# Optimization experiments

Hardware: AMD Instinct MI355X
Metric: run time of the kernel (lower is better)

Reference implementation:

```python
import jax, jax.numpy as jnp
import numpy as np


def setup_inputs() -> dict:
    key = jax.random.key(0)
    k1, k2, k3, k4, k5 = jax.random.split(key, 5)
    B, N, M, D = 4096, 2048, 2048, 9
    return {
        "x": jax.random.normal(k1, (B, N), dtype=jnp.float32),
        "eternal_weights": jax.random.normal(k2, (D, N, M), dtype=jnp.float32),
        "eternal_biases": jax.random.normal(k3, (M,), dtype=jnp.float32),
        "classical_weights": jax.random.normal(k4, (N, M), dtype=jnp.float32),
        "classical_biases": jax.random.normal(k5, (M,), dtype=jnp.float32),
    }


def _eternal_probs(eternal_weights, n, m):
    # The gate matrix is cos*I - sin*P + sin*P^T with P the circular shift,
    # so (gate @ s)[i] = cos*s[i] - sin*s[(i+1)%n] + sin*s[(i-1)%n].
    # Vectorize over all m output units at once: state is [m, n].
    state0 = jnp.full((m, n), 1.0 / np.sqrt(n), dtype=eternal_weights.dtype)
    angles = eternal_weights[:, :m, :3]  # [D, m, 3] -- weights[depth, j, 0/1/2]

    def gate(state, angle):  # angle: [m]
        c = jnp.cos(angle)[:, None]
        s = jnp.sin(angle)[:, None]
        return c * state - s * jnp.roll(state, -1, axis=1) + s * jnp.roll(state, 1, axis=1)

    def step(state, ang):  # ang: [m, 3] -- consciousness, intelligence, wisdom
        state = gate(state, ang[:, 0])
        state = gate(state, ang[:, 1])
        state = gate(state, ang[:, 2])
        return state, None

    state, _ = jax.lax.scan(step, state0, angles)
    return jnp.abs(state[:, 0]) ** 2  # [m]


def reference(x, eternal_weights, eternal_biases, classical_weights, classical_biases):
    # eternal_biases exists as a parameter in the original module but is unused in forward.
    n = x.shape[1]
    m = classical_weights.shape[1]
    classical = x @ classical_weights + classical_biases  # [B, m]
    probs = _eternal_probs(eternal_weights, n, m)  # [m], identical for every batch row
    return jnp.tanh(classical + probs[None, :])
```

## Files before the change

kernel.cpp:

```cpp
#include <hip/hip_runtime.h>
#include <hip/hip_fp8.h>
#include <stdint.h>

static constexpr int MM = 4096;
static constexpr int KK = 2048;
static constexpr int NN = 2048;

typedef float floatx16 __attribute__((ext_vector_type(16)));
typedef __bf16 bf16x8 __attribute__((ext_vector_type(8)));
typedef unsigned short u16x8 __attribute__((ext_vector_type(8)));
typedef int intx4 __attribute__((ext_vector_type(4)));
typedef int intx8 __attribute__((ext_vector_type(8)));
typedef unsigned char u8x16 __attribute__((ext_vector_type(16)));

__device__ __forceinline__ unsigned short bf16_rne(float x) {
  union { float f; uint32_t u; } c; c.f = x;
  uint32_t u = c.u;
  u += 0x7fffu + ((u >> 16) & 1u);
  return (unsigned short)(u >> 16);
}
__device__ __forceinline__ float bf16_as_f32(unsigned short h) {
  union { float f; uint32_t u; } c; c.u = ((uint32_t)h) << 16;
  return c.f;
}
__device__ __forceinline__ unsigned char f32_to_e4m3(float x) {
  __hip_fp8_e4m3 q(x);
  return (unsigned char)q.__x;
}
__device__ __forceinline__ float fast_tanh(float x) {
  float e = __expf(2.0f * x);
  return 1.0f - 2.0f / (e + 1.0f);
}
__device__ __forceinline__ float bflo(unsigned int w) {
  union { float f; unsigned u; } c; c.u = w << 16; return c.f;
}
__device__ __forceinline__ float bfhi(unsigned int w) {
  union { float f; unsigned u; } c; c.u = w & 0xffff0000u; return c.f;
}


__global__ __launch_bounds__(256) void prepass_kernel(
    const float* __restrict__ x, const float* __restrict__ E,
    const float* __restrict__ W, const float* __restrict__ cb,
    unsigned short* __restrict__ ahi, unsigned char* __restrict__ al8,
    unsigned short* __restrict__ bhi, unsigned char* __restrict__ bl8,
    float* __restrict__ bias2) {
  __shared__ float tile[64][65];
  const int blk = blockIdx.x;
  const int tid = threadIdx.x;

  if (blk < 2048) {
    int idx = blk * 256 + tid;
    int row = idx >> 7;
    int u = idx & 127;
    int g = u >> 2;
    int q = u & 3;
    const float4* s = (const float4*)(x + (size_t)row * KK + u * 16);
    float v[16];
#pragma unroll
    for (int p = 0; p < 4; p++) {
      float4 t = s[p];
      v[p * 4 + 0] = t.x; v[p * 4 + 1] = t.y; v[p * 4 + 2] = t.z; v[p * 4 + 3] = t.w;
    }
    unsigned short h[16];
    union { unsigned char b[16]; unsigned long long d[2]; } loq;
#pragma unroll
    for (int e = 0; e < 16; e++) {
      h[e] = bf16_rne(v[e]);
      float lo = v[e] - bf16_as_f32(h[e]);
      loq.b[e] = f32_to_e4m3(lo * 512.0f);
    }
    size_t rb = (size_t)row * KK;
#pragma unroll
    for (int cc = 0; cc < 2; cc++) {
      int c8 = q * 2 + cc;
      int phys8 = (c8 + row + (row >> 3)) & 7;
      u16x8 o;
#pragma unroll
      for (int e = 0; e < 8; e++) o[e] = h[cc * 8 + e];
      *(u16x8*)(ahi + rb + g * 64 + phys8 * 8) = o;
    }
    {
      int sw = (row & 3) + ((row >> 2) & 3);
      int cA = (q >> 1) * 2;
      char* lb = (char*)al8 + rb + g * 64;
      *(unsigned long long*)(lb + (((cA + 0) + sw) & 3) * 16 + (q & 1) * 8) = loq.d[0];
      *(unsigned long long*)(lb + (((cA + 1) + sw) & 3) * 16 + (q & 1) * 8) = loq.d[1];
    }
  } else if (blk < 3072) {
    const int wb = blk - 2048;
    const int n0 = (wb & 31) * 64;
    const int k0 = (wb >> 5) * 64;
#pragma unroll
    for (int i = 0; i < 4; i++) {
      int t = tid + i * 256;
      int kr = t >> 4;
      int nc = (t & 15) * 4;
      const float4 vv = *(const float4*)(W + (size_t)(k0 + kr) * NN + n0 + nc);
      tile[nc + 0][kr] = vv.x;
      tile[nc + 1][kr] = vv.y;
      tile[nc + 2][kr] = vv.z;
      tile[nc + 3][kr] = vv.w;
    }
    __syncthreads();
    const int nl = tid >> 2;
    const int q = tid & 3;
    const int n = n0 + nl;
    float v[16];
    unsigned short h[16];
    union { unsigned char b[16]; unsigned long long d[2]; } loq;
#pragma unroll
    for (int e = 0; e < 16; e++) {
      v[e] = tile[nl][q * 16 + e];
      h[e] = bf16_rne(v[e]);
      float lo = v[e] - bf16_as_f32(h[e]);
      loq.b[e] = f32_to_e4m3(lo * 512.0f);
    }
    size_t rb = (size_t)n * KK + k0;
#pragma unroll
    for (int cc = 0; cc < 2; cc++) {
      int c8 = q * 2 + cc;
      int phys8 = (c8 + n + (n >> 3)) & 7;
      u16x8 o;
#pragma unroll
      for (int e = 0; e < 8; e++) o[e] = h[cc * 8 + e];
      *(u16x8*)(bhi + rb + phys8 * 8) = o;
    }
    {
      int sw = (n & 3) + ((n >> 2) & 3);
      int cA = (q >> 1) * 2;
      char* lb = (char*)bl8 + rb;
      *(unsigned long long*)(lb + (((cA + 0) + sw) & 3) * 16 + (q & 1) * 8) = loq.d[0];
      *(unsigned long long*)(lb + (((cA + 1) + sw) & 3) * 16 + (q & 1) * 8) = loq.d[1];
    }
  } else {
    int i = (blk - 3072) * 256 + tid;
    if (i < NN) {
      float p = 1.0f / 2048.0f;
#pragma unroll
      for (int d = 0; d < 9; d++) {
        const float4 a = *(const float4*)(E + (size_t)d * (2048 * 2048) + (size_t)i * 2048);
        float c0 = cosf(a.x), c1 = cosf(a.y), c2 = cosf(a.z);
        p *= (c0 * c0) * (c1 * c1) * (c2 * c2);
      }
      bias2[i] = cb[i] + p;
    }
  }
}

#define GLL(dst, src)                                                        \
  __builtin_amdgcn_global_load_lds(                                          \
      (const __attribute__((address_space(1))) void*)(src),                  \
      (__attribute__((address_space(3))) void*)(dst), 16, 0, 0)

__global__ __launch_bounds__(256, 2) void gemm_tanh_kernel(
    const unsigned short* __restrict__ Ahi, const unsigned char* __restrict__ Al8,
    const unsigned short* __restrict__ Bhi, const unsigned char* __restrict__ Bl8,
    const float* __restrict__ bias2, float* __restrict__ out) {
  __shared__ __align__(16) unsigned short sAh[2][128 * 64];
  __shared__ __align__(16) unsigned short sBh[2][128 * 64];
  __shared__ __align__(16) unsigned char sAl[128 * 64];
  __shared__ __align__(16) unsigned char sBl[128 * 64];

  const int tid = threadIdx.x;
  const int lane = tid & 63;
  const int wave = tid >> 6;
  const int wm = (wave >> 1) * 64;
  const int wn = (wave & 1) * 64;

  const int id = blockIdx.x;
  const int cid = id >> 4, lid = id & 15;
  const int bm = ((cid >> 2) * 4 + (lid >> 2)) * 128;
  const int bn = ((cid & 3) * 4 + (lid & 3)) * 128;

  const size_t a16 = (size_t)(bm + (tid >> 3)) * KK + (tid & 7) * 8;
  const size_t b16 = (size_t)(bn + (tid >> 3)) * KK + (tid & 7) * 8;
  const size_t a8b = (size_t)(bm + (tid >> 2)) * KK + (tid & 3) * 16;
  const size_t b8b = (size_t)(bn + (tid >> 2)) * KK + (tid & 3) * 16;
  const int lds16 = tid * 8;
  const int lds8 = tid * 16;

  const int r31 = lane & 31;
  const int half = lane >> 5;

  floatx16 acc[2][2];
#pragma unroll
  for (int i = 0; i < 2; i++)
#pragma unroll
    for (int j = 0; j < 2; j++)
#pragma unroll
      for (int r = 0; r < 16; r++) acc[i][j][r] = 0.f;

#pragma unroll
  for (int p = 0; p < 4; p++) {
    GLL(&sAh[0][p * 2048 + lds16], Ahi + a16 + (size_t)(32 * p) * KK);
    GLL(&sBh[0][p * 2048 + lds16], Bhi + b16 + (size_t)(32 * p) * KK);
  }

  for (int kt = 0; kt < 32; ++kt) {
    const int k0 = kt * 64;
    const int cur = kt & 1;
    const int nxt = cur ^ 1;

    __builtin_amdgcn_s_barrier();
    __builtin_amdgcn_sched_barrier(0);
#pragma unroll
    for (int p = 0; p < 2; p++) {
      GLL(&sAl[p * 4096 + lds8], Al8 + a8b + (size_t)k0 + (size_t)(64 * p) * KK);
      GLL(&sBl[p * 4096 + lds8], Bl8 + b8b + (size_t)k0 + (size_t)(64 * p) * KK);
    }
    const size_t kn = (kt < 31) ? (size_t)(k0 + 64) : 0;
#pragma unroll
    for (int p = 0; p < 4; p++) {
      GLL(&sAh[nxt][p * 2048 + lds16], Ahi + a16 + kn + (size_t)(32 * p) * KK);
      GLL(&sBh[nxt][p * 2048 + lds16], Bhi + b16 + kn + (size_t)(32 * p) * KK);
    }
    asm volatile("s_waitcnt vmcnt(12)" ::: "memory");
    __builtin_amdgcn_sched_barrier(0);
    __builtin_amdgcn_s_barrier();
    __builtin_amdgcn_sched_barrier(0);

    intx8 fa8[2], fb8[2];
#pragma unroll
    for (int s = 0; s < 4; s++) {
      const int c8 = s * 2 + half;
      bf16x8 fa[2], fb[2];
#pragma unroll
      for (int t = 0; t < 2; t++) {
        int rowA = wm + t * 32 + r31;
        int ao = rowA * 64 + ((c8 + rowA + (rowA >> 3)) & 7) * 8;
        fa[t] = *(const bf16x8*)(&sAh[cur][ao]);
        int rowB = wn + t * 32 + r31;
        int bo = rowB * 64 + ((c8 + rowB + (rowB >> 3)) & 7) * 8;
        fb[t] = *(const bf16x8*)(&sBh[cur][bo]);
      }
#pragma unroll
      for (int i = 0; i < 2; i++)
#pragma unroll
        for (int j = 0; j < 2; j++)
          acc[i][j] = __builtin_amdgcn_mfma_f32_32x32x16_bf16(fa[i], fb[j], acc[i][j], 0, 0, 0);
#pragma unroll
      for (int t = 0; t < 2; t++) {
        uint4 ua = *(const uint4*)&fa[t];
        int d0 = __builtin_amdgcn_cvt_pk_fp8_f32(bflo(ua.x), bfhi(ua.x), 0, false);
        d0 = __builtin_amdgcn_cvt_pk_fp8_f32(bflo(ua.y), bfhi(ua.y), d0, true);
        int d1 = __builtin_amdgcn_cvt_pk_fp8_f32(bflo(ua.z), bfhi(ua.z), 0, false);
        d1 = __builtin_amdgcn_cvt_pk_fp8_f32(bflo(ua.w), bfhi(ua.w), d1, true);
        fa8[t][2 * s] = d0; fa8[t][2 * s + 1] = d1;
        uint4 ub = *(const uint4*)&fb[t];
        int e0 = __builtin_amdgcn_cvt_pk_fp8_f32(bflo(ub.x), bfhi(ub.x), 0, false);
        e0 = __builtin_amdgcn_cvt_pk_fp8_f32(bflo(ub.y), bfhi(ub.y), e0, true);
        int e1 = __builtin_amdgcn_cvt_pk_fp8_f32(bflo(ub.z), bfhi(ub.z), 0, false);
        e1 = __builtin_amdgcn_cvt_pk_fp8_f32(bflo(ub.w), bfhi(ub.w), e1, true);
        fb8[t][2 * s] = e0; fb8[t][2 * s + 1] = e1;
      }
    }

    asm volatile("s_waitcnt vmcnt(8)" ::: "memory");
    __builtin_amdgcn_sched_barrier(0);
    __builtin_amdgcn_s_barrier();
    __builtin_amdgcn_sched_barrier(0);

    intx8 fal[2], fbl[2];
#pragma unroll
    for (int t = 0; t < 2; t++) {
      int rowA = wm + t * 32 + r31;
      int swA = (rowA & 3) + ((rowA >> 2) & 3);
      ((intx4*)&fal[t])[0] = *(const intx4*)(&sAl[rowA * 64 + ((half + swA) & 3) * 16]);
      ((intx4*)&fal[t])[1] = *(const intx4*)(&sAl[rowA * 64 + ((2 + half + swA) & 3) * 16]);
      int rowB = wn + t * 32 + r31;
      int swB = (rowB & 3) + ((rowB >> 2) & 3);
      ((intx4*)&fbl[t])[0] = *(const intx4*)(&sBl[rowB * 64 + ((half + swB) & 3) * 16]);
      ((intx4*)&fbl[t])[1] = *(const intx4*)(&sBl[rowB * 64 + ((2 + half + swB) & 3) * 16]);
    }
#pragma unroll
    for (int i = 0; i < 2; i++)
#pragma unroll
      for (int j = 0; j < 2; j++)
        acc[i][j] = __builtin_amdgcn_mfma_scale_f32_32x32x64_f8f6f4(
            fal[i], fb8[j], acc[i][j], 0, 0, 0, 0x76767676, 0, 0x7f7f7f7f);
#pragma unroll
    for (int i = 0; i < 2; i++)
#pragma unroll
      for (int j = 0; j < 2; j++)
        acc[i][j] = __builtin_amdgcn_mfma_scale_f32_32x32x64_f8f6f4(
            fa8[i], fbl[j], acc[i][j], 0, 0, 0, 0x7f7f7f7f, 0, 0x76767676);
  }

#pragma unroll
  for (int j = 0; j < 2; j++) {
    int col = bn + wn + j * 32 + r31;
    float b2 = bias2[col];
#pragma unroll
    for (int i = 0; i < 2; i++) {
      int row0 = bm + wm + i * 32 + 4 * half;
#pragma unroll
      for (int r = 0; r < 16; r++) {
        int row = row0 + (r & 3) + 8 * (r >> 2);
        float val = acc[i][j][r] + b2;
        __builtin_nontemporal_store(fast_tanh(val), &out[(size_t)row * NN + col]);
      }
    }
  }
}

__global__ __launch_bounds__(256) void fallback_gemm(
    const float* __restrict__ x, const float* __restrict__ E,
    const float* __restrict__ W, const float* __restrict__ cb,
    float* __restrict__ out) {
  __shared__ float sA[16][16];
  __shared__ float sB[16][17];
  __shared__ float sbias[16];
  const int tx = threadIdx.x, ty = threadIdx.y;
  const int row = blockIdx.y * 16 + ty;
  const int col = blockIdx.x * 16 + tx;
  if (ty == 0) {
    float p = 1.0f / 2048.0f;
    for (int d = 0; d < 9; d++) {
      const float* a = E + (size_t)d * (2048 * 2048) + (size_t)col * 2048;
      for (int t = 0; t < 3; t++) { float c = cosf(a[t]); p *= c * c; }
    }
    sbias[tx] = p + cb[col];
  }
  float acc = 0.f;
  for (int k0 = 0; k0 < KK; k0 += 16) {
    __syncthreads();
    sA[ty][tx] = x[(size_t)row * KK + k0 + tx];
    sB[ty][tx] = W[(size_t)(k0 + ty) * NN + col];
    __syncthreads();
#pragma unroll
    for (int kk = 0; kk < 16; kk++) acc += sA[ty][kk] * sB[kk][tx];
  }
  out[(size_t)row * NN + col] = tanhf(acc + sbias[tx]);
}

extern "C" void kernel_launch(void* const* d_in, const int* in_sizes, int n_in,
                              void* d_out, int out_size, void* d_ws, size_t ws_size,
                              hipStream_t stream) {
  const float* x  = (const float*)d_in[0];
  const float* E  = (const float*)d_in[1];
  const float* W  = (const float*)d_in[3];
  const float* cb = (const float*)d_in[4];
  float* out = (float*)d_out;

  const size_t MB = 1024 * 1024;
  const size_t need = 36 * MB + NN * sizeof(float);
  if (ws_size < need) {
    fallback_gemm<<<dim3(NN / 16, MM / 16), dim3(16, 16), 0, stream>>>(x, E, W, cb, out);
    return;
  }

  char* ws = (char*)d_ws;
  unsigned short* Ahi = (unsigned short*)(ws);
  unsigned short* Bhi = (unsigned short*)(ws + 16 * MB);
  unsigned char* Al8  = (unsigned char*)(ws + 24 * MB);
  unsigned char* Bl8  = (unsigned char*)(ws + 32 * MB);
  float* bias2 = (float*)(ws + 36 * MB);

  prepass_kernel<<<dim3(3080), dim3(256), 0, stream>>>(
      x, E, W, cb, Ahi, Al8, Bhi, Bl8, bias2);
  gemm_tanh_kernel<<<dim3(512), dim3(256), 0, stream>>>(
      Ahi, Al8, Bhi, Bl8, bias2, out);
}
```

Measured before the change: 308.3 us.

## Switch split-precision GEMM from bf16 to fp16 hi part with perm-based fp8 cross terms

Replaces the bf16 high part with fp16 and rescales the fp8 residual (x2048, scale exponent adjusted). The cross-term operands are now taken as the high byte of each fp16 via byte permutes, read as the bf8 format, instead of eight cvt_pk_fp8 conversions per fragment. The change also unrolls the k-loop by two with static buffer indices, precomputes LDS offsets, and raises wave priority around the MFMA sections. This aims to cut VALU conversion and address work in the inner loop, at the risk of fp16 range and accuracy limits.

```diff
diff --git a/kernel.cpp b/kernel.cpp
--- a/kernel.cpp
+++ b/kernel.cpp
@@ -7,22 +7,11 @@
 static constexpr int NN = 2048;
 
 typedef float floatx16 __attribute__((ext_vector_type(16)));
-typedef __bf16 bf16x8 __attribute__((ext_vector_type(8)));
+typedef _Float16 f16x8 __attribute__((ext_vector_type(8)));
 typedef unsigned short u16x8 __attribute__((ext_vector_type(8)));
 typedef int intx4 __attribute__((ext_vector_type(4)));
 typedef int intx8 __attribute__((ext_vector_type(8)));
-typedef unsigned char u8x16 __attribute__((ext_vector_type(16)));
-
-__device__ __forceinline__ unsigned short bf16_rne(float x) {
-  union { float f; uint32_t u; } c; c.f = x;
-  uint32_t u = c.u;
-  u += 0x7fffu + ((u >> 16) & 1u);
-  return (unsigned short)(u >> 16);
-}
-__device__ __forceinline__ float bf16_as_f32(unsigned short h) {
-  union { float f; uint32_t u; } c; c.u = ((uint32_t)h) << 16;
-  return c.f;
-}
+
 __device__ __forceinline__ unsigned char f32_to_e4m3(float x) {
   __hip_fp8_e4m3 q(x);
   return (unsigned char)q.__x;
@@ -31,11 +20,13 @@
   float e = __expf(2.0f * x);
   return 1.0f - 2.0f / (e + 1.0f);
 }
-__device__ __forceinline__ float bflo(unsigned int w) {
-  union { float f; unsigned u; } c; c.u = w << 16; return c.f;
-}
-__device__ __forceinline__ float bfhi(unsigned int w) {
-  union { float f; unsigned u; } c; c.u = w & 0xffff0000u; return c.f;
+__device__ __forceinline__ unsigned short f32_to_f16_bits(float x) {
+  union { _Float16 h; unsigned short u; } c; c.h = (_Float16)x;
+  return c.u;
+}
+__device__ __forceinline__ float f16_bits_to_f32(unsigned short u) {
+  union { _Float16 h; unsigned short u; } c; c.u = u;
+  return (float)c.h;
 }
 
 
@@ -66,9 +57,9 @@
     union { unsigned char b[16]; unsigned long long d[2]; } loq;
 #pragma unroll
     for (int e = 0; e < 16; e++) {
-      h[e] = bf16_rne(v[e]);
-      float lo = v[e] - bf16_as_f32(h[e]);
-      loq.b[e] = f32_to_e4m3(lo * 512.0f);
+      h[e] = f32_to_f16_bits(v[e]);
+      float lo = v[e] - f16_bits_to_f32(h[e]);
+      loq.b[e] = f32_to_e4m3(lo * 2048.0f);
     }
     size_t rb = (size_t)row * KK;
 #pragma unroll
@@ -112,9 +103,9 @@
 #pragma unroll
     for (int e = 0; e < 16; e++) {
       v[e] = tile[nl][q * 16 + e];
-      h[e] = bf16_rne(v[e]);
-      float lo = v[e] - bf16_as_f32(h[e]);
-      loq.b[e] = f32_to_e4m3(lo * 512.0f);
+      h[e] = f32_to_f16_bits(v[e]);
+      float lo = v[e] - f16_bits_to_f32(h[e]);
+      loq.b[e] = f32_to_e4m3(lo * 2048.0f);
     }
     size_t rb = (size_t)n * KK + k0;
 #pragma unroll
@@ -153,14 +144,74 @@
       (const __attribute__((address_space(1))) void*)(src),                  \
       (__attribute__((address_space(3))) void*)(dst), 16, 0, 0)
 
+#define BODY(CUR, NXT, KLO, KNX)                                               \
+  {                                                                            \
+    __builtin_amdgcn_s_barrier();                                              \
+    __builtin_amdgcn_sched_barrier(0);                                         \
+    _Pragma("unroll") for (int p = 0; p < 2; p++) {                            \
+      GLL(&sAl[p * 4096 + lds8], Al8 + a8b + (size_t)(KLO) + (size_t)(64 * p) * KK); \
+      GLL(&sBl[p * 4096 + lds8], Bl8 + b8b + (size_t)(KLO) + (size_t)(64 * p) * KK); \
+    }                                                                          \
+    _Pragma("unroll") for (int p = 0; p < 4; p++) {                            \
+      GLL(&sAh[NXT][p * 2048 + lds16], Ahi + a16 + (size_t)(KNX) + (size_t)(32 * p) * KK); \
+      GLL(&sBh[NXT][p * 2048 + lds16], Bhi + b16 + (size_t)(KNX) + (size_t)(32 * p) * KK); \
+    }                                                                          \
+    asm volatile("s_waitcnt vmcnt(12)" ::: "memory");                          \
+    __builtin_amdgcn_sched_barrier(0);                                         \
+    __builtin_amdgcn_s_barrier();                                              \
+    __builtin_amdgcn_sched_barrier(0);                                         \
+    intx8 fa8[2], fb8[2];                                                      \
+    __builtin_amdgcn_s_setprio(1);                                             \
+    _Pragma("unroll") for (int s = 0; s < 4; s++) {                            \
+      f16x8 fa[2], fb[2];                                                      \
+      _Pragma("unroll") for (int t = 0; t < 2; t++) {                          \
+        fa[t] = *(const f16x8*)(sAhB + (CUR) * 16384 + aho[s][t]);             \
+        fb[t] = *(const f16x8*)(sBhB + (CUR) * 16384 + bho[s][t]);             \
+      }                                                                        \
+      _Pragma("unroll") for (int i = 0; i < 2; i++)                            \
+        _Pragma("unroll") for (int j = 0; j < 2; j++)                          \
+          acc[i][j] = __builtin_amdgcn_mfma_f32_32x32x16_f16(fa[i], fb[j], acc[i][j], 0, 0, 0); \
+      _Pragma("unroll") for (int t = 0; t < 2; t++) {                          \
+        const uint4 ua = *(const uint4*)&fa[t];                                \
+        fa8[t][2 * s]     = (int)__builtin_amdgcn_perm(ua.y, ua.x, 0x07050301u); \
+        fa8[t][2 * s + 1] = (int)__builtin_amdgcn_perm(ua.w, ua.z, 0x07050301u); \
+        const uint4 ub = *(const uint4*)&fb[t];                                \
+        fb8[t][2 * s]     = (int)__builtin_amdgcn_perm(ub.y, ub.x, 0x07050301u); \
+        fb8[t][2 * s + 1] = (int)__builtin_amdgcn_perm(ub.w, ub.z, 0x07050301u); \
+      }                                                                        \
+    }                                                                          \
+    __builtin_amdgcn_s_setprio(0);                                             \
+    asm volatile("s_waitcnt vmcnt(8)" ::: "memory");                           \
+    __builtin_amdgcn_sched_barrier(0);                                         \
+    __builtin_amdgcn_s_barrier();                                              \
+    __builtin_amdgcn_sched_barrier(0);                                         \
+    intx8 fal[2], fbl[2];                                                      \
+    _Pragma("unroll") for (int t = 0; t < 2; t++) {                            \
+      ((intx4*)&fal[t])[0] = *(const intx4*)(sAlB + alo[t][0]);                \
+      ((intx4*)&fal[t])[1] = *(const intx4*)(sAlB + alo[t][1]);                \
+      ((intx4*)&fbl[t])[0] = *(const intx4*)(sBlB + blo[t][0]);                \
+      ((intx4*)&fbl[t])[1] = *(const intx4*)(sBlB + blo[t][1]);                \
+    }                                                                          \
+    __builtin_amdgcn_s_setprio(1);                                             \
+    _Pragma("unroll") for (int i = 0; i < 2; i++)                              \
+      _Pragma("unroll") for (int j = 0; j < 2; j++)                            \
+        acc[i][j] = __builtin_amdgcn_mfma_scale_f32_32x32x64_f8f6f4(           \
+            fal[i], fb8[j], acc[i][j], 0, 1, 0, 0x74747474, 0, 0x7f7f7f7f);    \
+    _Pragma("unroll") for (int i = 0; i < 2; i++)                              \
+      _Pragma("unroll") for (int j = 0; j < 2; j++)                            \
+        acc[i][j] = __builtin_amdgcn_mfma_scale_f32_32x32x64_f8f6f4(           \
+            fa8[i], fbl[j], acc[i][j], 1, 0, 0, 0x7f7f7f7f, 0, 0x74747474);    \
+    __builtin_amdgcn_s_setprio(0);                                             \
+  }
+
 __global__ __launch_bounds__(256, 2) void gemm_tanh_kernel(
     const unsigned short* __restrict__ Ahi, const unsigned char* __restrict__ Al8,
     const unsigned short* __restrict__ Bhi, const unsigned char* __restrict__ Bl8,
     const float* __restrict__ bias2, float* __restrict__ out) {
-  __shared__ __align__(16) unsigned short sAh[2][128 * 64];
-  __shared__ __align__(16) unsigned short sBh[2][128 * 64];
-  __shared__ __align__(16) unsigned char sAl[128 * 64];
-  __shared__ __align__(16) unsigned char sBl[128 * 64];
+  __shared__ __align__(16) unsigned short sAh[2][8192];
+  __shared__ __align__(16) unsigned short sBh[2][8192];
+  __shared__ __align__(16) unsigned char sAl[8192];
+  __shared__ __align__(16) unsigned char sBl[8192];
 
   const int tid = threadIdx.x;
   const int lane = tid & 63;
@@ -183,6 +234,33 @@
   const int r31 = lane & 31;
   const int half = lane >> 5;
 
+  const char* sAhB = (const char*)(&sAh[0][0]);
+  const char* sBhB = (const char*)(&sBh[0][0]);
+  const char* sAlB = (const char*)(&sAl[0]);
+  const char* sBlB = (const char*)(&sBl[0]);
+  int aho[4][2], bho[4][2];
+#pragma unroll
+  for (int s = 0; s < 4; s++)
+#pragma unroll
+    for (int t = 0; t < 2; t++) {
+      const int rowA = wm + t * 32 + r31;
+      aho[s][t] = rowA * 128 + ((2 * s + half + rowA + (rowA >> 3)) & 7) * 16;
+      const int rowB = wn + t * 32 + r31;
+      bho[s][t] = rowB * 128 + ((2 * s + half + rowB + (rowB >> 3)) & 7) * 16;
+    }
+  int alo[2][2], blo[2][2];
+#pragma unroll
+  for (int t = 0; t < 2; t++) {
+    const int rowA = wm + t * 32 + r31;
+    const int swA = (rowA & 3) + ((rowA >> 2) & 3);
+    alo[t][0] = rowA * 64 + ((half + swA) & 3) * 16;
+    alo[t][1] = rowA * 64 + ((2 + half + swA) & 3) * 16;
+    const int rowB = wn + t * 32 + r31;
+    const int swB = (rowB & 3) + ((rowB >> 2) & 3);
+    blo[t][0] = rowB * 64 + ((half + swB) & 3) * 16;
+    blo[t][1] = rowB * 64 + ((2 + half + swB) & 3) * 16;
+  }
+
   floatx16 acc[2][2];
 #pragma unroll
   for (int i = 0; i < 2; i++)
@@ -197,95 +275,12 @@
     GLL(&sBh[0][p * 2048 + lds16], Bhi + b16 + (size_t)(32 * p) * KK);
   }
 
-  for (int kt = 0; kt < 32; ++kt) {
+  for (int kt = 0; kt < 32; kt += 2) {
     const int k0 = kt * 64;
-    const int cur = kt & 1;
-    const int nxt = cur ^ 1;
-
-    __builtin_amdgcn_s_barrier();
-    __builtin_amdgcn_sched_barrier(0);
-#pragma unroll
-    for (int p = 0; p < 2; p++) {
-      GLL(&sAl[p * 4096 + lds8], Al8 + a8b + (size_t)k0 + (size_t)(64 * p) * KK);
-      GLL(&sBl[p * 4096 + lds8], Bl8 + b8b + (size_t)k0 + (size_t)(64 * p) * KK);
-    }
-    const size_t kn = (kt < 31) ? (size_t)(k0 + 64) : 0;
-#pragma unroll
-    for (int p = 0; p < 4; p++) {
-      GLL(&sAh[nxt][p * 2048 + lds16], Ahi + a16 + kn + (size_t)(32 * p) * KK);
-      GLL(&sBh[nxt][p * 2048 + lds16], Bhi + b16 + kn + (size_t)(32 * p) * KK);
-    }
-    asm volatile("s_waitcnt vmcnt(12)" ::: "memory");
-    __builtin_amdgcn_sched_barrier(0);
-    __builtin_amdgcn_s_barrier();
-    __builtin_amdgcn_sched_barrier(0);
-
-    intx8 fa8[2], fb8[2];
-#pragma unroll
-    for (int s = 0; s < 4; s++) {
-      const int c8 = s * 2 + half;
-      bf16x8 fa[2], fb[2];
-#pragma unroll
-      for (int t = 0; t < 2; t++) {
-        int rowA = wm + t * 32 + r31;
-        int ao = rowA * 64 + ((c8 + rowA + (rowA >> 3)) & 7) * 8;
-        fa[t] = *(const bf16x8*)(&sAh[cur][ao]);
-        int rowB = wn + t * 32 + r31;
-        int bo = rowB * 64 + ((c8 + rowB + (rowB >> 3)) & 7) * 8;
-        fb[t] = *(const bf16x8*)(&sBh[cur][bo]);
-      }
-#pragma unroll
-      for (int i = 0; i < 2; i++)
-#pragma unroll
-        for (int j = 0; j < 2; j++)
-          acc[i][j] = __builtin_amdgcn_mfma_f32_32x32x16_bf16(fa[i], fb[j], acc[i][j], 0, 0, 0);
-#pragma unroll
-      for (int t = 0; t < 2; t++) {
-        uint4 ua = *(const uint4*)&fa[t];
-        int d0 = __builtin_amdgcn_cvt_pk_fp8_f32(bflo(ua.x), bfhi(ua.x), 0, false);
-        d0 = __builtin_amdgcn_cvt_pk_fp8_f32(bflo(ua.y), bfhi(ua.y), d0, true);
-        int d1 = __builtin_amdgcn_cvt_pk_fp8_f32(bflo(ua.z), bfhi(ua.z), 0, false);
-        d1 = __builtin_amdgcn_cvt_pk_fp8_f32(bflo(ua.w), bfhi(ua.w), d1, true);
-        fa8[t][2 * s] = d0; fa8[t][2 * s + 1] = d1;
-        uint4 ub = *(const uint4*)&fb[t];
-        int e0 = __builtin_amdgcn_cvt_pk_fp8_f32(bflo(ub.x), bfhi(ub.x), 0, false);
-        e0 = __builtin_amdgcn_cvt_pk_fp8_f32(bflo(ub.y), bfhi(ub.y), e0, true);
-        int e1 = __builtin_amdgcn_cvt_pk_fp8_f32(bflo(ub.z), bfhi(ub.z), 0, false);
-        e1 = __builtin_amdgcn_cvt_pk_fp8_f32(bflo(ub.w), bfhi(ub.w), e1, true);
-        fb8[t][2 * s] = e0; fb8[t][2 * s + 1] = e1;
-      }
-    }
-
-    asm volatile("s_waitcnt vmcnt(8)" ::: "memory");
-    __builtin_amdgcn_sched_barrier(0);
-    __builtin_amdgcn_s_barrier();
-    __builtin_amdgcn_sched_barrier(0);
-
-    intx8 fal[2], fbl[2];
-#pragma unroll
-    for (int t = 0; t < 2; t++) {
-      int rowA = wm + t * 32 + r31;
-      int swA = (rowA & 3) + ((rowA >> 2) & 3);
-      ((intx4*)&fal[t])[0] = *(const intx4*)(&sAl[rowA * 64 + ((half + swA) & 3) * 16]);
-      ((intx4*)&fal[t])[1] = *(const intx4*)(&sAl[rowA * 64 + ((2 + half + swA) & 3) * 16]);
-      int rowB = wn + t * 32 + r31;
-      int swB = (rowB & 3) + ((rowB >> 2) & 3);
-      ((intx4*)&fbl[t])[0] = *(const intx4*)(&sBl[rowB * 64 + ((half + swB) & 3) * 16]);
-      ((intx4*)&fbl[t])[1] = *(const intx4*)(&sBl[rowB * 64 + ((2 + half + swB) & 3) * 16]);
-    }
-#pragma unroll
-    for (int i = 0; i < 2; i++)
-#pragma unroll
-      for (int j = 0; j < 2; j++)
-        acc[i][j] = __builtin_amdgcn_mfma_scale_f32_32x32x64_f8f6f4(
-            fal[i], fb8[j], acc[i][j], 0, 0, 0, 0x76767676, 0, 0x7f7f7f7f);
-#pragma unroll
-    for (int i = 0; i < 2; i++)
-#pragma unroll
-      for (int j = 0; j < 2; j++)
-        acc[i][j] = __builtin_amdgcn_mfma_scale_f32_32x32x64_f8f6f4(
-            fa8[i], fbl[j], acc[i][j], 0, 0, 0, 0x7f7f7f7f, 0, 0x76767676);
-  }
+    BODY(0, 1, k0, k0 + 64)
+    BODY(1, 0, k0 + 64, (kt < 30) ? (k0 + 128) : 0)
+  }
+  asm volatile("s_waitcnt vmcnt(0)" ::: "memory");
 
 #pragma unroll
   for (int j = 0; j < 2; j++) {
```

After: 295.0 us. -4.3%, faster.

## Switch to fp16 hi split with MFMA-fragment layout and direct global loads

Applied to the files above, without the earlier changes.

The prepass now splits inputs into fp16 high parts plus e4m3 residuals scaled by 2048, and writes them in a tiled layout that matches the MFMA fragment order. The GEMM kernel drops the LDS staging and barriers and loads fragments straight from global memory into registers. It also gets the fp8 copy of the high part by byte-permuting fp16 into bf8 instead of running float conversions, and raises wave priority around the MFMA blocks. The risks are the loss of prefetch double-buffering, which can expose global latency, and the narrower fp16 exponent range for the high part.

```diff
diff --git a/kernel.cpp b/kernel.cpp
--- a/kernel.cpp
+++ b/kernel.cpp
@@ -7,22 +7,11 @@
 static constexpr int NN = 2048;
 
 typedef float floatx16 __attribute__((ext_vector_type(16)));
-typedef __bf16 bf16x8 __attribute__((ext_vector_type(8)));
+typedef _Float16 f16x8 __attribute__((ext_vector_type(8)));
 typedef unsigned short u16x8 __attribute__((ext_vector_type(8)));
 typedef int intx4 __attribute__((ext_vector_type(4)));
 typedef int intx8 __attribute__((ext_vector_type(8)));
-typedef unsigned char u8x16 __attribute__((ext_vector_type(16)));
-
-__device__ __forceinline__ unsigned short bf16_rne(float x) {
-  union { float f; uint32_t u; } c; c.f = x;
-  uint32_t u = c.u;
-  u += 0x7fffu + ((u >> 16) & 1u);
-  return (unsigned short)(u >> 16);
-}
-__device__ __forceinline__ float bf16_as_f32(unsigned short h) {
-  union { float f; uint32_t u; } c; c.u = ((uint32_t)h) << 16;
-  return c.f;
-}
+
 __device__ __forceinline__ unsigned char f32_to_e4m3(float x) {
   __hip_fp8_e4m3 q(x);
   return (unsigned char)q.__x;
@@ -31,11 +20,13 @@
   float e = __expf(2.0f * x);
   return 1.0f - 2.0f / (e + 1.0f);
 }
-__device__ __forceinline__ float bflo(unsigned int w) {
-  union { float f; unsigned u; } c; c.u = w << 16; return c.f;
-}
-__device__ __forceinline__ float bfhi(unsigned int w) {
-  union { float f; unsigned u; } c; c.u = w & 0xffff0000u; return c.f;
+__device__ __forceinline__ unsigned short f32_to_f16_bits(float x) {
+  union { _Float16 h; unsigned short u; } c; c.h = (_Float16)x;
+  return c.u;
+}
+__device__ __forceinline__ float f16_bits_to_f32(unsigned short u) {
+  union { _Float16 h; unsigned short u; } c; c.u = u;
+  return (float)c.h;
 }
 
 
@@ -66,31 +57,29 @@
     union { unsigned char b[16]; unsigned long long d[2]; } loq;
 #pragma unroll
     for (int e = 0; e < 16; e++) {
-      h[e] = bf16_rne(v[e]);
-      float lo = v[e] - bf16_as_f32(h[e]);
-      loq.b[e] = f32_to_e4m3(lo * 512.0f);
-    }
-    size_t rb = (size_t)row * KK;
+      h[e] = f32_to_f16_bits(v[e]);
+      float lo = v[e] - f16_bits_to_f32(h[e]);
+      loq.b[e] = f32_to_e4m3(lo * 2048.0f);
+    }
+    char* ah = (char*)ahi + (size_t)(row >> 5) * 131072 + (size_t)g * 4096 + (row & 31) * 16;
 #pragma unroll
     for (int cc = 0; cc < 2; cc++) {
-      int c8 = q * 2 + cc;
-      int phys8 = (c8 + row + (row >> 3)) & 7;
       u16x8 o;
 #pragma unroll
       for (int e = 0; e < 8; e++) o[e] = h[cc * 8 + e];
-      *(u16x8*)(ahi + rb + g * 64 + phys8 * 8) = o;
+      *(u16x8*)(ah + (2 * q + cc) * 512) = o;
     }
     {
-      int sw = (row & 3) + ((row >> 2) & 3);
-      int cA = (q >> 1) * 2;
-      char* lb = (char*)al8 + rb + g * 64;
-      *(unsigned long long*)(lb + (((cA + 0) + sw) & 3) * 16 + (q & 1) * 8) = loq.d[0];
-      *(unsigned long long*)(lb + (((cA + 1) + sw) & 3) * 16 + (q & 1) * 8) = loq.d[1];
+      char* al = (char*)al8 + (size_t)(row >> 5) * 65536 + (size_t)g * 2048 +
+                 (row & 31) * 16 + (q & 1) * 8;
+      *(unsigned long long*)(al + (q & 2) * 512) = loq.d[0];
+      *(unsigned long long*)(al + ((q & 2) | 1) * 512) = loq.d[1];
     }
   } else if (blk < 3072) {
     const int wb = blk - 2048;
     const int n0 = (wb & 31) * 64;
     const int k0 = (wb >> 5) * 64;
+    const int g = wb >> 5;
 #pragma unroll
     for (int i = 0; i < 4; i++) {
       int t = tid + i * 256;
@@ -112,26 +101,23 @@
 #pragma unroll
     for (int e = 0; e < 16; e++) {
       v[e] = tile[nl][q * 16 + e];
-      h[e] = bf16_rne(v[e]);
-      float lo = v[e] - bf16_as_f32(h[e]);
-      loq.b[e] = f32_to_e4m3(lo * 512.0f);
-    }
-    size_t rb = (size_t)n * KK + k0;
+      h[e] = f32_to_f16_bits(v[e]);
+      float lo = v[e] - f16_bits_to_f32(h[e]);
+      loq.b[e] = f32_to_e4m3(lo * 2048.0f);
+    }
+    char* bh = (char*)bhi + (size_t)(n >> 5) * 131072 + (size_t)g * 4096 + (n & 31) * 16;
 #pragma unroll
     for (int cc = 0; cc < 2; cc++) {
-      int c8 = q * 2 + cc;
-      int phys8 = (c8 + n + (n >> 3)) & 7;
       u16x8 o;
 #pragma unroll
       for (int e = 0; e < 8; e++) o[e] = h[cc * 8 + e];
-      *(u16x8*)(bhi + rb + phys8 * 8) = o;
+      *(u16x8*)(bh + (2 * q + cc) * 512) = o;
     }
     {
-      int sw = (n & 3) + ((n >> 2) & 3);
-      int cA = (q >> 1) * 2;
-      char* lb = (char*)bl8 + rb;
-      *(unsigned long long*)(lb + (((cA + 0) + sw) & 3) * 16 + (q & 1) * 8) = loq.d[0];
-      *(unsigned long long*)(lb + (((cA + 1) + sw) & 3) * 16 + (q & 1) * 8) = loq.d[1];
+      char* bl = (char*)bl8 + (size_t)(n >> 5) * 65536 + (size_t)g * 2048 +
+                 (n & 31) * 16 + (q & 1) * 8;
+      *(unsigned long long*)(bl + (q & 2) * 512) = loq.d[0];
+      *(unsigned long long*)(bl + ((q & 2) | 1) * 512) = loq.d[1];
     }
   } else {
     int i = (blk - 3072) * 256 + tid;
@@ -148,20 +134,13 @@
   }
 }
 
-#define GLL(dst, src)                                                        \
-  __builtin_amdgcn_global_load_lds(                                          \
-      (const __attribute__((address_space(1))) void*)(src),                  \
-      (__attribute__((address_space(3))) void*)(dst), 16, 0, 0)
+#define GLDH(p) (*(const __attribute__((address_space(1))) f16x8*)(p))
+#define GLD4(p) (*(const __attribute__((address_space(1))) intx4*)(p))
 
 __global__ __launch_bounds__(256, 2) void gemm_tanh_kernel(
     const unsigned short* __restrict__ Ahi, const unsigned char* __restrict__ Al8,
     const unsigned short* __restrict__ Bhi, const unsigned char* __restrict__ Bl8,
     const float* __restrict__ bias2, float* __restrict__ out) {
-  __shared__ __align__(16) unsigned short sAh[2][128 * 64];
-  __shared__ __align__(16) unsigned short sBh[2][128 * 64];
-  __shared__ __align__(16) unsigned char sAl[128 * 64];
-  __shared__ __align__(16) unsigned char sBl[128 * 64];
-
   const int tid = threadIdx.x;
   const int lane = tid & 63;
   const int wave = tid >> 6;
@@ -173,16 +152,20 @@
   const int bm = ((cid >> 2) * 4 + (lid >> 2)) * 128;
   const int bn = ((cid & 3) * 4 + (lid & 3)) * 128;
 
-  const size_t a16 = (size_t)(bm + (tid >> 3)) * KK + (tid & 7) * 8;
-  const size_t b16 = (size_t)(bn + (tid >> 3)) * KK + (tid & 7) * 8;
-  const size_t a8b = (size_t)(bm + (tid >> 2)) * KK + (tid & 3) * 16;
-  const size_t b8b = (size_t)(bn + (tid >> 2)) * KK + (tid & 3) * 16;
-  const int lds16 = tid * 8;
-  const int lds8 = tid * 16;
-
   const int r31 = lane & 31;
   const int half = lane >> 5;
 
+  const char* aH[2]; const char* bH[2]; const char* aL[2]; const char* bL[2];
+#pragma unroll
+  for (int t = 0; t < 2; t++) {
+    const size_t Ta = (size_t)((bm + wm + 32 * t) >> 5);
+    aH[t] = (const char*)Ahi + Ta * 131072 + half * 512 + r31 * 16;
+    aL[t] = (const char*)Al8 + Ta * 65536 + half * 512 + r31 * 16;
+    const size_t Tb = (size_t)((bn + wn + 32 * t) >> 5);
+    bH[t] = (const char*)Bhi + Tb * 131072 + half * 512 + r31 * 16;
+    bL[t] = (const char*)Bl8 + Tb * 65536 + half * 512 + r31 * 16;
+  }
+
   floatx16 acc[2][2];
 #pragma unroll
   for (int i = 0; i < 2; i++)
@@ -191,100 +174,75 @@
 #pragma unroll
       for (int r = 0; r < 16; r++) acc[i][j][r] = 0.f;
 
-#pragma unroll
-  for (int p = 0; p < 4; p++) {
-    GLL(&sAh[0][p * 2048 + lds16], Ahi + a16 + (size_t)(32 * p) * KK);
-    GLL(&sBh[0][p * 2048 + lds16], Bhi + b16 + (size_t)(32 * p) * KK);
-  }
-
-  for (int kt = 0; kt < 32; ++kt) {
-    const int k0 = kt * 64;
-    const int cur = kt & 1;
-    const int nxt = cur ^ 1;
-
-    __builtin_amdgcn_s_barrier();
-    __builtin_amdgcn_sched_barrier(0);
-#pragma unroll
-    for (int p = 0; p < 2; p++) {
-      GLL(&sAl[p * 4096 + lds8], Al8 + a8b + (size_t)k0 + (size_t)(64 * p) * KK);
-      GLL(&sBl[p * 4096 + lds8], Bl8 + b8b + (size_t)k0 + (size_t)(64 * p) * KK);
-    }
-    const size_t kn = (kt < 31) ? (size_t)(k0 + 64) : 0;
-#pragma unroll
-    for (int p = 0; p < 4; p++) {
-      GLL(&sAh[nxt][p * 2048 + lds16], Ahi + a16 + kn + (size_t)(32 * p) * KK);
-      GLL(&sBh[nxt][p * 2048 + lds16], Bhi + b16 + kn + (size_t)(32 * p) * KK);
-    }
-    asm volatile("s_waitcnt vmcnt(12)" ::: "memory");
-    __builtin_amdgcn_sched_barrier(0);
-    __builtin_amdgcn_s_barrier();
-    __builtin_amdgcn_sched_barrier(0);
+  for (int g = 0; g < 32; ++g) {
+    f16x8 fa[4][2], fb[4][2];
+#pragma unroll
+    for (int s = 0; s < 4; s++)
+#pragma unroll
+      for (int t = 0; t < 2; t++) {
+        fa[s][t] = GLDH(aH[t] + s * 1024);
+        fb[s][t] = GLDH(bH[t] + s * 1024);
+      }
+    intx4 la[2][2], lb[2][2];
+#pragma unroll
+    for (int t = 0; t < 2; t++)
+#pragma unroll
+      for (int c = 0; c < 2; c++) {
+        la[t][c] = GLD4(aL[t] + c * 1024);
+        lb[t][c] = GLD4(bL[t] + c * 1024);
+      }
+
+    __builtin_amdgcn_s_setprio(1);
+#pragma unroll
+    for (int s = 0; s < 4; s++)
+#pragma unroll
+      for (int i = 0; i < 2; i++)
+#pragma unroll
+        for (int j = 0; j < 2; j++)
+          acc[i][j] = __builtin_amdgcn_mfma_f32_32x32x16_f16(fa[s][i], fb[s][j], acc[i][j], 0, 0, 0);
+    __builtin_amdgcn_s_setprio(0);
 
     intx8 fa8[2], fb8[2];
 #pragma unroll
-    for (int s = 0; s < 4; s++) {
-      const int c8 = s * 2 + half;
-      bf16x8 fa[2], fb[2];
+    for (int s = 0; s < 4; s++)
 #pragma unroll
       for (int t = 0; t < 2; t++) {
-        int rowA = wm + t * 32 + r31;
-        int ao = rowA * 64 + ((c8 + rowA + (rowA >> 3)) & 7) * 8;
-        fa[t] = *(const bf16x8*)(&sAh[cur][ao]);
-        int rowB = wn + t * 32 + r31;
-        int bo = rowB * 64 + ((c8 + rowB + (rowB >> 3)) & 7) * 8;
-        fb[t] = *(const bf16x8*)(&sBh[cur][bo]);
-      }
-#pragma unroll
-      for (int i = 0; i < 2; i++)
-#pragma unroll
-        for (int j = 0; j < 2; j++)
-          acc[i][j] = __builtin_amdgcn_mfma_f32_32x32x16_bf16(fa[i], fb[j], acc[i][j], 0, 0, 0);
-#pragma unroll
-      for (int t = 0; t < 2; t++) {
-        uint4 ua = *(const uint4*)&fa[t];
-        int d0 = __builtin_amdgcn_cvt_pk_fp8_f32(bflo(ua.x), bfhi(ua.x), 0, false);
-        d0 = __builtin_amdgcn_cvt_pk_fp8_f32(bflo(ua.y), bfhi(ua.y), d0, true);
-        int d1 = __builtin_amdgcn_cvt_pk_fp8_f32(bflo(ua.z), bfhi(ua.z), 0, false);
-        d1 = __builtin_amdgcn_cvt_pk_fp8_f32(bflo(ua.w), bfhi(ua.w), d1, true);
-        fa8[t][2 * s] = d0; fa8[t][2 * s + 1] = d1;
-        uint4 ub = *(const uint4*)&fb[t];
-        int e0 = __builtin_amdgcn_cvt_pk_fp8_f32(bflo(ub.x), bfhi(ub.x), 0, false);
-        e0 = __builtin_amdgcn_cvt_pk_fp8_f32(bflo(ub.y), bfhi(ub.y), e0, true);
-        int e1 = __builtin_amdgcn_cvt_pk_fp8_f32(bflo(ub.z), bfhi(ub.z), 0, false);
-        e1 = __builtin_amdgcn_cvt_pk_fp8_f32(bflo(ub.w), bfhi(ub.w), e1, true);
-        fb8[t][2 * s] = e0; fb8[t][2 * s + 1] = e1;
-      }
-    }
-
-    asm volatile("s_waitcnt vmcnt(8)" ::: "memory");
-    __builtin_amdgcn_sched_barrier(0);
-    __builtin_amdgcn_s_barrier();
-    __builtin_amdgcn_sched_barrier(0);
-
+        const uint4 ua = *(const uint4*)&fa[s][t];
+        fa8[t][2 * s]     = (int)__builtin_amdgcn_perm(ua.y, ua.x, 0x07050301u);
+        fa8[t][2 * s + 1] = (int)__builtin_amdgcn_perm(ua.w, ua.z, 0x07050301u);
+        const uint4 ub = *(const uint4*)&fb[s][t];
+        fb8[t][2 * s]     = (int)__builtin_amdgcn_perm(ub.y, ub.x, 0x07050301u);
+        fb8[t][2 * s + 1] = (int)__builtin_amdgcn_perm(ub.w, ub.z, 0x07050301u);
+      }
     intx8 fal[2], fbl[2];
 #pragma unroll
     for (int t = 0; t < 2; t++) {
-      int rowA = wm + t * 32 + r31;
-      int swA = (rowA & 3) + ((rowA >> 2) & 3);
-      ((intx4*)&fal[t])[0] = *(const intx4*)(&sAl[rowA * 64 + ((half + swA) & 3) * 16]);
-      ((intx4*)&fal[t])[1] = *(const intx4*)(&sAl[rowA * 64 + ((2 + half + swA) & 3) * 16]);
-      int rowB = wn + t * 32 + r31;
-      int swB = (rowB & 3) + ((rowB >> 2) & 3);
-      ((intx4*)&fbl[t])[0] = *(const intx4*)(&sBl[rowB * 64 + ((half + swB) & 3) * 16]);
-      ((intx4*)&fbl[t])[1] = *(const intx4*)(&sBl[rowB * 64 + ((2 + half + swB) & 3) * 16]);
-    }
+      ((intx4*)&fal[t])[0] = la[t][0];
+      ((intx4*)&fal[t])[1] = la[t][1];
+      ((intx4*)&fbl[t])[0] = lb[t][0];
+      ((intx4*)&fbl[t])[1] = lb[t][1];
+    }
+
+    __builtin_amdgcn_s_setprio(1);
 #pragma unroll
     for (int i = 0; i < 2; i++)
 #pragma unroll
       for (int j = 0; j < 2; j++)
         acc[i][j] = __builtin_amdgcn_mfma_scale_f32_32x32x64_f8f6f4(
-            fal[i], fb8[j], acc[i][j], 0, 0, 0, 0x76767676, 0, 0x7f7f7f7f);
+            fal[i], fb8[j], acc[i][j], 0, 1, 0, 0x74747474, 0, 0x7f7f7f7f);
 #pragma unroll
     for (int i = 0; i < 2; i++)
 #pragma unroll
       for (int j = 0; j < 2; j++)
         acc[i][j] = __builtin_amdgcn_mfma_scale_f32_32x32x64_f8f6f4(
-            fa8[i], fbl[j], acc[i][j], 0, 0, 0, 0x7f7f7f7f, 0, 0x76767676);
+            fa8[i], fbl[j], acc[i][j], 1, 0, 0, 0x7f7f7f7f, 0, 0x74747474);
+    __builtin_amdgcn_s_setprio(0);
+
+#pragma unroll
+    for (int t = 0; t < 2; t++) {
+      aH[t] += 4096; bH[t] += 4096;
+      aL[t] += 2048; bL[t] += 2048;
+    }
   }
 
 #pragma unroll
```

Measured after the change: 311.1 us. No clear change (+0.9%).
